# Performance work log

Measured on AMD Instinct MI355X. Metric: run time of the kernel, lower is better.

Reference implementation:

```python
import jax, jax.numpy as jnp
import numpy as np

B, L, D = 2, 2048, 2048
N, K, H = 16, 8, 128
EPS = 1e-6
ROPE_THETA = 1000000
K_MASK = -2.3819763e+38


def rms_norm(x, w, eps=EPS):
    dtype = x.dtype
    rms = jnp.sqrt(jnp.mean(x.astype(jnp.float32) ** 2, axis=-1, keepdims=True) + eps)
    return (w * x / rms).astype(dtype)


def apply_rope(inputs, positions, head_dim, rope_theta=ROPE_THETA):
    # inputs: [B, L, n, H], positions: [B, L]
    fraction = 2 * jnp.arange(0, head_dim // 2, dtype=jnp.float32) / head_dim
    timescale = rope_theta ** fraction  # [H/2]
    sinusoid = positions[..., jnp.newaxis] / timescale[jnp.newaxis, jnp.newaxis, :]  # [B,L,H/2]
    sinusoid = sinusoid[..., jnp.newaxis, :]  # [B,L,1,H/2]
    sin, cos = jnp.sin(sinusoid), jnp.cos(sinusoid)
    first, second = jnp.split(inputs, 2, axis=-1)
    out = jnp.concatenate([first * cos - second * sin, second * cos + first * sin], axis=-1)
    return out.astype(inputs.dtype)


def setup_inputs() -> dict:
    key = jax.random.key(0)
    ks = jax.random.split(key, 6)
    x = jax.random.normal(ks[0], (B, L, D), dtype=jnp.float32)
    position_ids = jnp.broadcast_to(jnp.arange(L, dtype=jnp.int32)[None, :], (B, L))
    # causal mask [B, L, S]
    attn_mask = jnp.broadcast_to(jnp.tril(jnp.ones((L, L), dtype=bool))[None], (B, L, L))
    wq = jax.random.normal(ks[1], (D, N, H), dtype=jnp.float32) * 0.02
    wk = jax.random.normal(ks[2], (D, K, H), dtype=jnp.float32) * 0.02
    wv = jax.random.normal(ks[3], (D, K, H), dtype=jnp.float32) * 0.02
    wo = jax.random.normal(ks[4], (N, H, D), dtype=jnp.float32) * 0.02
    q_norm_w = jnp.ones((H,), dtype=jnp.float32)
    k_norm_w = jnp.ones((H,), dtype=jnp.float32)
    return {"x": x, "position_ids": position_ids, "attn_mask": attn_mask,
            "wq": wq, "wk": wk, "wv": wv, "wo": wo,
            "q_norm_w": q_norm_w, "k_norm_w": k_norm_w}


def reference(x, position_ids, attn_mask, wq, wk, wv, wo, q_norm_w, k_norm_w):
    scale = H ** (-0.5)
    q = jnp.einsum('BLD,DNH->BLNH', x, wq)  # [B,L,N,H]
    k = jnp.einsum('BSD,DKH->BSKH', x, wk)  # [B,S,K,H]
    v = jnp.einsum('BSD,DKH->BSKH', x, wv)
    q = rms_norm(q, q_norm_w)
    k = rms_norm(k, k_norm_w)
    q = apply_rope(q, position_ids, H)
    k = apply_rope(k, position_ids, H)
    b, l, n, h = q.shape
    s = k.shape[1]
    kk = k.shape[2]
    q = q.reshape((b, l, kk, n // kk, h))
    attn = jnp.einsum('BLKGH,BSKH->BKGLS', q, k) * scale
    attn = attn.reshape((b, n, l, s))
    attn = jnp.where(jnp.expand_dims(attn_mask, -3), attn, K_MASK)
    attn = jax.nn.softmax(attn.astype(jnp.float32), axis=-1).astype(k.dtype)
    attn = attn.reshape((b, kk, n // kk, l, s))
    qkv = jnp.einsum('BKGLS,BSKH->BLKGH', attn, v).reshape((b, l, n, h))
    out = jnp.einsum('BLNH,NHD->BLD', qkv, wo)
    return out
```

## Files before the change

### kernel.cpp

```cpp
#include <hip/hip_runtime.h>
#include <hip/hip_bf16.h>

#define B_ 2
#define L_ 2048
#define D_ 2048
#define NH_ 16
#define KH_ 8
#define HD_ 128

typedef __attribute__((ext_vector_type(8))) short short8;
typedef __attribute__((ext_vector_type(4))) short short4v;
typedef __attribute__((ext_vector_type(4))) float floatx4;

__device__ __forceinline__ unsigned short f2bf(float f) {
  unsigned u = __float_as_uint(f);
  unsigned r = (u + 0x7fffu + ((u >> 16) & 1u)) >> 16;
  return (unsigned short)r;
}
__device__ __forceinline__ float bf2f(unsigned short h) {
  return __uint_as_float(((unsigned)h) << 16);
}
__device__ __forceinline__ unsigned pack_bf16x2(float a, float b) {
  __hip_bfloat162 h = __float22bfloat162_rn(make_float2(a, b));
  return *reinterpret_cast<unsigned*>(&h);
}
__device__ __forceinline__ void gl_lds16(const void* g, void* l) {
  __builtin_amdgcn_global_load_lds(
      (const __attribute__((address_space(1))) unsigned int*)g,
      (__attribute__((address_space(3))) unsigned int*)l, 16, 0, 0);
}
__device__ __forceinline__ void barrier_lds_only() {
  asm volatile("s_waitcnt lgkmcnt(0)" ::: "memory");
  __builtin_amdgcn_s_barrier();
}

__global__ __launch_bounds__(256) void prep1(const float* __restrict__ x,
                                             const float* __restrict__ wq,
                                             const float* __restrict__ wk,
                                             const float* __restrict__ wv,
                                             const float* __restrict__ wo,
                                             unsigned short* __restrict__ xb,
                                             unsigned short* __restrict__ wqkv_t,
                                             unsigned short* __restrict__ wo_t) {
  int id = blockIdx.x;
  int t = threadIdx.x;
  if (id < 8192) {
    long i = ((long)id * 256 + t) * 4;
    float4 v = *(const float4*)(x + i);
    ushort4 o;
    o.x = f2bf(v.x); o.y = f2bf(v.y); o.z = f2bf(v.z); o.w = f2bf(v.w);
    *(ushort4*)(xb + i) = o;
    return;
  }
  id -= 8192;
  __shared__ float tile[32][33];
  const float* in;
  unsigned short* out;
  int C, sh;
  if (id < 4096) {
    in = wq; out = wqkv_t; C = 2048; sh = 6;
  } else if (id < 6144) {
    in = wk; out = wqkv_t + 2048L * 2048; C = 1024; sh = 5; id -= 4096;
  } else if (id < 8192) {
    in = wv; out = wqkv_t + 3072L * 2048; C = 1024; sh = 5; id -= 6144;
  } else {
    in = wo; out = wo_t; C = 2048; sh = 6; id -= 8192;
  }
  int c0 = (id & ((1 << sh) - 1)) * 32, r0 = (id >> sh) * 32;
  int tx = t & 31, ty = t >> 5;
#pragma unroll
  for (int i = 0; i < 4; i++)
    tile[ty + i * 8][tx] = in[(long)(r0 + ty + i * 8) * C + c0 + tx];
  __syncthreads();
#pragma unroll
  for (int i = 0; i < 4; i++) {
    int oc = ty + i * 8;
    out[(long)(c0 + oc) * 2048 + r0 + tx] = f2bf(tile[tx][oc]);
  }
}

__global__ __launch_bounds__(256) void prep2(const unsigned short* __restrict__ qkv,
                                             const int* __restrict__ pos,
                                             const float* __restrict__ qw,
                                             const float* __restrict__ kw,
                                             unsigned short* __restrict__ qo,
                                             unsigned short* __restrict__ ko,
                                             unsigned short* __restrict__ vT) {
  int id = blockIdx.x;
  int t = threadIdx.x;
  if (id < 24576) {
    const int lane = t & 63, w = t >> 6;
    const int gid = id * 4 + w;
    const int row = gid / 24;
    const int hd = gid - row * 24;
    const int b = row >> 11, l = row & 2047;
    const unsigned short* src = qkv + (long)row * 4096 + hd * 128;
    float x0 = bf2f(src[lane]);
    float x1 = bf2f(src[lane + 64]);
    float ss = x0 * x0 + x1 * x1;
#pragma unroll
    for (int off = 32; off; off >>= 1) ss += __shfl_xor(ss, off);
    float inv = 1.0f / sqrtf(ss * (1.0f / 128.0f) + 1e-6f);
    const float* nw = (hd < 16) ? qw : kw;
    x0 = nw[lane] * x0 * inv;
    x1 = nw[lane + 64] * x1 * inv;
    float p = (float)pos[row];
    float ang = p * exp2f((float)lane * -0.31143075889f);
    float s, c;
    sincosf(ang, &s, &c);
    float o0 = x0 * c - x1 * s;
    float o1 = x1 * c + x0 * s;
    unsigned short* dst;
    if (hd < 16) {
      const float QSC = 0.08838834764831845f * 1.4426950408889634f;
      o0 *= QSC;
      o1 *= QSC;
      dst = qo + (((long)b * NH_ + hd) * L_ + l) * HD_;
    } else {
      dst = ko + (((long)b * KH_ + (hd - 16)) * L_ + l) * HD_;
    }
    dst[lane] = f2bf(o0);
    dst[lane + 64] = f2bf(o1);
    return;
  }
  id -= 24576;
  __shared__ unsigned short tile[32][33];
  int l0 = (id & 63) * 32, h0 = ((id >> 6) & 3) * 32;
  int bk = id >> 8;
  int b = bk >> 3, kh = bk & 7;
  int tx = t & 31, ty = t >> 5;
  const unsigned short* src = qkv + (long)b * L_ * 4096 + 3072 + kh * 128;
#pragma unroll
  for (int i = 0; i < 4; i++)
    tile[ty + i * 8][tx] = src[(long)(l0 + ty + i * 8) * 4096 + h0 + tx];
  __syncthreads();
  unsigned short* dst = vT + (long)bk * HD_ * L_;
#pragma unroll
  for (int i = 0; i < 4; i++)
    dst[(long)(h0 + ty + i * 8) * L_ + l0 + tx] = tile[tx][ty + i * 8];
}

template <int MODE>
__global__ __launch_bounds__(256, 3) void gemm128(const unsigned short* __restrict__ A,
                                                  const unsigned short* __restrict__ Bt,
                                                  void* __restrict__ C,
                                                  int M, int N, int K) {
  __shared__ unsigned short As[128 * 64];
  __shared__ unsigned short Bs[128 * 64];
  const int t = threadIdx.x;
  const int lane = t & 63, w = t >> 6;
  const int wy = w >> 1, wx = w & 1;
  const int col = lane & 15, quad = lane >> 4;
  const long m0 = (long)blockIdx.y * 128, n0 = (long)blockIdx.x * 128;
  floatx4 acc[4][4];
#pragma unroll
  for (int i = 0; i < 4; i++)
#pragma unroll
    for (int j = 0; j < 4; j++) acc[i][j] = (floatx4)0.0f;
  const int rs = t >> 3, bs = t & 7;
  for (int kt = 0; kt < K; kt += 64) {
#pragma unroll
    for (int i = 0; i < 4; i++) {
      int r = i * 32 + rs;
      gl_lds16(A + (m0 + r) * (long)K + kt + ((bs ^ (r & 7)) << 3),
               &As[(i * 32 + w * 8) * 64]);
      gl_lds16(Bt + (n0 + r) * (long)K + kt + ((bs ^ (r & 7)) << 3),
               &Bs[(i * 32 + w * 8) * 64]);
    }
    __syncthreads();
#pragma unroll
    for (int ks = 0; ks < 2; ks++) {
      short8 af[4], bf[4];
#pragma unroll
      for (int mi = 0; mi < 4; mi++) {
        int row = wy * 64 + mi * 16 + col;
        int blk = ks * 4 + quad;
        af[mi] = *(const short8*)&As[row * 64 + ((blk ^ (row & 7)) << 3)];
      }
#pragma unroll
      for (int ni = 0; ni < 4; ni++) {
        int row = wx * 64 + ni * 16 + col;
        int blk = ks * 4 + quad;
        bf[ni] = *(const short8*)&Bs[row * 64 + ((blk ^ (row & 7)) << 3)];
      }
#pragma unroll
      for (int mi = 0; mi < 4; mi++)
#pragma unroll
        for (int ni = 0; ni < 4; ni++)
          acc[mi][ni] = __builtin_amdgcn_mfma_f32_16x16x32_bf16(af[mi], bf[ni],
                                                                acc[mi][ni], 0, 0, 0);
    }
    __syncthreads();
  }
#pragma unroll
  for (int mi = 0; mi < 4; mi++)
#pragma unroll
    for (int r = 0; r < 4; r++) {
      long row = m0 + wy * 64 + mi * 16 + quad * 4 + r;
#pragma unroll
      for (int ni = 0; ni < 4; ni++) {
        long cg = n0 + wx * 64 + ni * 16 + col;
        float val = acc[mi][ni][r];
        if (MODE == 1)
          ((unsigned short*)C)[row * N + cg] = f2bf(val);
        else
          ((float*)C)[row * N + cg] = val;
      }
    }
}

template <int MODE>
__global__ __launch_bounds__(512, 2) void gemm256(const unsigned short* __restrict__ A,
                                                  const unsigned short* __restrict__ Bt,
                                                  void* __restrict__ C,
                                                  int M, int N, int K) {
  __shared__ unsigned short As[2][256 * 64];
  __shared__ unsigned short Bs[2][256 * 64];
  const int t = threadIdx.x;
  const int lane = t & 63, w = t >> 6;
  const int wy = w >> 2, wx = w & 3;
  const int col = lane & 15, quad = lane >> 4;
  const long m0 = (long)blockIdx.y * 256, n0 = (long)blockIdx.x * 256;
  const int rs = t >> 3, bs = t & 7;
  const int nt = K >> 6;

#define SA256(bufi, Tt, h)                                                      \
  gl_lds16(A + (m0 + (h) * 64 + rs) * (long)K + (long)(Tt) * 64 +               \
               ((bs ^ (rs & 7)) << 3),                                          \
           &As[bufi][((h) * 64 + w * 8) * 64])
#define SB256(bufi, Tt, h)                                                      \
  gl_lds16(Bt + (n0 + (h) * 64 + rs) * (long)K + (long)(Tt) * 64 +              \
                ((bs ^ (rs & 7)) << 3),                                         \
           &Bs[bufi][((h) * 64 + w * 8) * 64])

  floatx4 acc[8][4];
#pragma unroll
  for (int i = 0; i < 8; i++)
#pragma unroll
    for (int j = 0; j < 4; j++) acc[i][j] = (floatx4)0.0f;

  SA256(0, 0, 0); SA256(0, 0, 1); SA256(0, 0, 2); SA256(0, 0, 3);
  SB256(0, 0, 0); SB256(0, 0, 1); SB256(0, 0, 2); SB256(0, 0, 3);
  SB256(1, 1, 0); SB256(1, 1, 1); SB256(1, 1, 2); SB256(1, 1, 3);
  asm volatile("s_waitcnt vmcnt(4)" ::: "memory");
  __builtin_amdgcn_s_barrier();

  for (int T = 0; T < nt; ++T) {
    const int c = T & 1;
    const unsigned short* Ac = As[c];
    const unsigned short* Bc = Bs[c];
    short8 a[4][2], b[4][2];

#pragma unroll
    for (int mi = 0; mi < 4; mi++)
#pragma unroll
      for (int ks = 0; ks < 2; ks++) {
        int row = wy * 128 + mi * 16 + col;
        a[mi][ks] = *(const short8*)&Ac[row * 64 + (((ks * 4 + quad) ^ (row & 7)) << 3)];
      }
#pragma unroll
    for (int ni = 0; ni < 2; ni++)
#pragma unroll
      for (int ks = 0; ks < 2; ks++) {
        int row = wx * 64 + ni * 16 + col;
        b[ni][ks] = *(const short8*)&Bc[row * 64 + (((ks * 4 + quad) ^ (row & 7)) << 3)];
      }
    if (T + 1 < nt) { SA256(c ^ 1, T + 1, 0); SA256(c ^ 1, T + 1, 2); }
    __builtin_amdgcn_s_barrier();
    asm volatile("s_waitcnt lgkmcnt(0)" ::: "memory");
    __builtin_amdgcn_s_setprio(1);
#pragma unroll
    for (int mi = 0; mi < 4; mi++)
#pragma unroll
      for (int ni = 0; ni < 2; ni++)
#pragma unroll
        for (int ks = 0; ks < 2; ks++)
          acc[mi][ni] = __builtin_amdgcn_mfma_f32_16x16x32_bf16(a[mi][ks], b[ni][ks],
                                                                acc[mi][ni], 0, 0, 0);
    __builtin_amdgcn_s_setprio(0);
    __builtin_amdgcn_s_barrier();

#pragma unroll
    for (int ni = 2; ni < 4; ni++)
#pragma unroll
      for (int ks = 0; ks < 2; ks++) {
        int row = wx * 64 + ni * 16 + col;
        b[ni][ks] = *(const short8*)&Bc[row * 64 + (((ks * 4 + quad) ^ (row & 7)) << 3)];
      }
    if (T + 1 < nt) { SA256(c ^ 1, T + 1, 1); SA256(c ^ 1, T + 1, 3); }
    __builtin_amdgcn_s_barrier();
    asm volatile("s_waitcnt lgkmcnt(0)" ::: "memory");
    __builtin_amdgcn_s_setprio(1);
#pragma unroll
    for (int mi = 0; mi < 4; mi++)
#pragma unroll
      for (int ni = 2; ni < 4; ni++)
#pragma unroll
        for (int ks = 0; ks < 2; ks++)
          acc[mi][ni] = __builtin_amdgcn_mfma_f32_16x16x32_bf16(a[mi][ks], b[ni][ks],
                                                                acc[mi][ni], 0, 0, 0);
    __builtin_amdgcn_s_setprio(0);
    __builtin_amdgcn_s_barrier();

#pragma unroll
    for (int mi = 0; mi < 4; mi++)
#pragma unroll
      for (int ks = 0; ks < 2; ks++) {
        int row = wy * 128 + (mi + 4) * 16 + col;
        a[mi][ks] = *(const short8*)&Ac[row * 64 + (((ks * 4 + quad) ^ (row & 7)) << 3)];
      }
    if (T + 2 < nt) { SB256(c, T + 2, 0); SB256(c, T + 2, 1); }
    __builtin_amdgcn_s_barrier();
    asm volatile("s_waitcnt lgkmcnt(0)" ::: "memory");
    __builtin_amdgcn_s_setprio(1);
#pragma unroll
    for (int mi = 0; mi < 4; mi++)
#pragma unroll
      for (int ni = 0; ni < 2; ni++)
#pragma unroll
        for (int ks = 0; ks < 2; ks++)
          acc[mi + 4][ni] = __builtin_amdgcn_mfma_f32_16x16x32_bf16(a[mi][ks], b[ni][ks],
                                                                    acc[mi + 4][ni], 0, 0, 0);
    __builtin_amdgcn_s_setprio(0);
    __builtin_amdgcn_s_barrier();

    if (T + 2 < nt) { SB256(c, T + 2, 2); SB256(c, T + 2, 3); }
    __builtin_amdgcn_s_setprio(1);
#pragma unroll
    for (int mi = 0; mi < 4; mi++)
#pragma unroll
      for (int ni = 2; ni < 4; ni++)
#pragma unroll
        for (int ks = 0; ks < 2; ks++)
          acc[mi + 4][ni] = __builtin_amdgcn_mfma_f32_16x16x32_bf16(a[mi][ks], b[ni][ks],
                                                                    acc[mi + 4][ni], 0, 0, 0);
    __builtin_amdgcn_s_setprio(0);
    if (T + 1 < nt) {
      if (T >= nt - 2)
        asm volatile("s_waitcnt vmcnt(0)" ::: "memory");
      else
        asm volatile("s_waitcnt vmcnt(4)" ::: "memory");
      __builtin_amdgcn_s_barrier();
    }
  }
#undef SA256
#undef SB256

#pragma unroll
  for (int mi = 0; mi < 8; mi++)
#pragma unroll
    for (int r = 0; r < 4; r++) {
      long row = m0 + wy * 128 + mi * 16 + quad * 4 + r;
#pragma unroll
      for (int ni = 0; ni < 4; ni++) {
        long cg = n0 + wx * 64 + ni * 16 + col;
        float val = acc[mi][ni][r];
        if (MODE == 1)
          ((unsigned short*)C)[row * N + cg] = f2bf(val);
        else
          ((float*)C)[row * N + cg] = val;
      }
    }
}

__global__ __launch_bounds__(256, 2) void flash(const unsigned short* __restrict__ Q,
                                                const unsigned short* __restrict__ Kg,
                                                const unsigned short* __restrict__ VT,
                                                unsigned short* __restrict__ Og) {
  __shared__ unsigned short Ks[64 * 128];
  __shared__ unsigned short Vs[128 * 64];
  __shared__ unsigned short Ps[128 * 72];
  const int n = blockIdx.y, b = blockIdx.z;
  const int qt = b ? (15 - blockIdx.x) : blockIdx.x;
  const int t = threadIdx.x, lane = t & 63, w = t >> 6;
  const int col = lane & 15, quad = lane >> 4;
  const int kvh = n >> 1;
  const unsigned short* kb = Kg + ((long)b * KH_ + kvh) * L_ * HD_;
  const unsigned short* vtb = VT + ((long)b * KH_ + kvh) * HD_ * L_;
  const int l0 = qt * 128;
  const int steps = 2 * qt + 2;
  const unsigned short* qb = Q + (((long)b * NH_ + n) * L_ + l0) * HD_;

  const int rK = t >> 4, blkK = t & 15;
  const int rV = t >> 3, blkV = t & 7;

  short8 qf[2][4];
#pragma unroll
  for (int mi = 0; mi < 2; mi++)
#pragma unroll
    for (int ks = 0; ks < 4; ks++)
      qf[mi][ks] = *(const short8*)(qb + (w * 32 + mi * 16 + col) * 128 + ks * 32 + quad * 8);

  floatx4 o[2][8];
#pragma unroll
  for (int mi = 0; mi < 2; mi++)
#pragma unroll
    for (int nf = 0; nf < 8; nf++) o[mi][nf] = (floatx4)0.0f;
  float lrowA[2] = {0.0f, 0.0f}, lrowB[2] = {0.0f, 0.0f};

  {
#pragma unroll
    for (int i = 0; i < 4; i++) {
      int r = i * 16 + rK;
      int gblk = (blkK & 8) | ((blkK ^ r) & 7);
      gl_lds16(kb + (long)r * 128 + gblk * 8, &Ks[(i * 16 + w * 4) * 128]);
    }
#pragma unroll
    for (int j = 0; j < 4; j++) {
      int r = j * 32 + rV;
      int gblk = (blkV ^ r) & 7;
      gl_lds16(vtb + (long)r * L_ + gblk * 8, &Vs[(j * 32 + w * 8) * 64]);
    }
  }
  __syncthreads();

  short8 kpre[4], vpre[4];
  if (steps > 1) {
    const int s0n = 64;
#pragma unroll
    for (int i = 0; i < 4; i++) {
      int r = i * 16 + rK;
      int gblk = (blkK & 8) | ((blkK ^ r) & 7);
      kpre[i] = *(const short8*)(kb + (long)(s0n + r) * 128 + gblk * 8);
    }
#pragma unroll
    for (int j = 0; j < 4; j++) {
      int r = j * 32 + rV;
      int gblk = (blkV ^ r) & 7;
      vpre[j] = *(const short8*)(vtb + (long)r * L_ + s0n + gblk * 8);
    }
  }

  for (int st = 0; st < steps; st++) {
    const int s0 = st * 64;

    floatx4 sa[2][4];
#pragma unroll
    for (int mi = 0; mi < 2; mi++)
#pragma unroll
      for (int sf = 0; sf < 4; sf++) sa[mi][sf] = (floatx4)0.0f;
#pragma unroll
    for (int ks = 0; ks < 4; ks++) {
      short8 bf[4];
#pragma unroll
      for (int sf = 0; sf < 4; sf++) {
        int srow = sf * 16 + col;
        int blk = ks * 4 + quad;
        bf[sf] = *(const short8*)&Ks[srow * 128 + (((blk & 8) | ((blk ^ srow) & 7)) << 3)];
      }
#pragma unroll
      for (int mi = 0; mi < 2; mi++)
#pragma unroll
        for (int sf = 0; sf < 4; sf++)
          sa[mi][sf] = __builtin_amdgcn_mfma_f32_16x16x32_bf16(bf[sf], qf[mi][ks],
                                                               sa[mi][sf], 0, 0, 0);
    }

    if (st >= steps - 2) {
#pragma unroll
      for (int mi = 0; mi < 2; mi++) {
        int lg = l0 + w * 32 + mi * 16 + col;
#pragma unroll
        for (int sf = 0; sf < 4; sf++)
#pragma unroll
          for (int r = 0; r < 4; r++) {
            int sg = s0 + sf * 16 + quad * 4 + r;
            if (sg > lg) sa[mi][sf][r] = -3.0e38f;
          }
      }
    }

#pragma unroll
    for (int mi = 0; mi < 2; mi++)
#pragma unroll
      for (int sf = 0; sf < 4; sf++) {
        float p0 = exp2f(sa[mi][sf][0] - 17.0f);
        float p1 = exp2f(sa[mi][sf][1] - 17.0f);
        float p2 = exp2f(sa[mi][sf][2] - 17.0f);
        float p3 = exp2f(sa[mi][sf][3] - 17.0f);
        lrowA[mi] += p0 + p1;
        lrowB[mi] += p2 + p3;
        uint2 pk;
        pk.x = pack_bf16x2(p0, p1);
        pk.y = pack_bf16x2(p2, p3);
        *(uint2*)&Ps[(w * 32 + mi * 16 + col) * 72 + sf * 16 + quad * 4] = pk;
      }

#pragma unroll
    for (int ks = 0; ks < 2; ks++) {
      short8 pf[2];
#pragma unroll
      for (int mi = 0; mi < 2; mi++)
        pf[mi] = *(const short8*)&Ps[(w * 32 + mi * 16 + col) * 72 + ks * 32 + quad * 8];
      short8 vf[8];
#pragma unroll
      for (int nf = 0; nf < 8; nf++) {
        int h = nf * 16 + col;
        int blk = ks * 4 + quad;
        vf[nf] = *(const short8*)&Vs[h * 64 + ((blk ^ (h & 7)) << 3)];
      }
#pragma unroll
      for (int mi = 0; mi < 2; mi++)
#pragma unroll
        for (int nf = 0; nf < 8; nf++)
          o[mi][nf] = __builtin_amdgcn_mfma_f32_16x16x32_bf16(pf[mi], vf[nf],
                                                              o[mi][nf], 0, 0, 0);
    }

    barrier_lds_only();
    if (st + 1 < steps) {
#pragma unroll
      for (int i = 0; i < 4; i++) {
        int r = i * 16 + rK;
        *(short8*)&Ks[r * 128 + blkK * 8] = kpre[i];
      }
#pragma unroll
      for (int j = 0; j < 4; j++) {
        int r = j * 32 + rV;
        *(short8*)&Vs[r * 64 + blkV * 8] = vpre[j];
      }
      barrier_lds_only();
      if (st + 2 < steps) {
        const int s0n = (st + 2) * 64;
#pragma unroll
        for (int i = 0; i < 4; i++) {
          int r = i * 16 + rK;
          int gblk = (blkK & 8) | ((blkK ^ r) & 7);
          kpre[i] = *(const short8*)(kb + (long)(s0n + r) * 128 + gblk * 8);
        }
#pragma unroll
        for (int j = 0; j < 4; j++) {
          int r = j * 32 + rV;
          int gblk = (blkV ^ r) & 7;
          vpre[j] = *(const short8*)(vtb + (long)r * L_ + s0n + gblk * 8);
        }
      }
    }
  }

#pragma unroll
  for (int mi = 0; mi < 2; mi++) {
    float s = lrowA[mi] + lrowB[mi];
    s += __shfl_xor(s, 16);
    s += __shfl_xor(s, 32);
#pragma unroll
    for (int r = 0; r < 4; r++) {
      float inv = 1.0f / __shfl(s, quad * 4 + r);
      int lg = l0 + w * 32 + mi * 16 + quad * 4 + r;
      unsigned short* dst = Og + (((long)b * L_ + lg) * NH_ + n) * HD_;
#pragma unroll
      for (int nf = 0; nf < 8; nf++)
        dst[nf * 16 + col] = f2bf(o[mi][nf][r] * inv);
    }
  }
}

extern "C" void kernel_launch(void* const* d_in, const int* in_sizes, int n_in,
                              void* d_out, int out_size, void* d_ws, size_t ws_size,
                              hipStream_t stream) {
  const float* x = (const float*)d_in[0];
  const int* pos = (const int*)d_in[1];
  const float* wq = (const float*)d_in[3];
  const float* wk = (const float*)d_in[4];
  const float* wv = (const float*)d_in[5];
  const float* wo = (const float*)d_in[6];
  const float* qnw = (const float*)d_in[7];
  const float* knw = (const float*)d_in[8];
  float* out = (float*)d_out;

  char* ws = (char*)d_ws;
  unsigned short* xb     = (unsigned short*)(ws + 0);
  unsigned short* wqkv_t = (unsigned short*)(ws + 16777216);
  unsigned short* wo_t   = (unsigned short*)(ws + 33554432);
  unsigned short* qkv    = (unsigned short*)(ws + 41943040);
  unsigned short* q      = (unsigned short*)(ws + 75497472);
  unsigned short* k      = (unsigned short*)(ws + 92274688);
  unsigned short* vT     = (unsigned short*)(ws + 100663296);
  unsigned short* ao     = (unsigned short*)(ws + 109051904);
  if (ws_size < 125829120) return;

  prep1<<<20480, 256, 0, stream>>>(x, wq, wk, wv, wo, xb, wqkv_t, wo_t);
  gemm256<1><<<dim3(16, 16), 512, 0, stream>>>(xb, wqkv_t, qkv, 4096, 4096, 2048);
  prep2<<<28672, 256, 0, stream>>>(qkv, pos, qnw, knw, q, k, vT);
  flash<<<dim3(16, NH_, B_), 256, 0, stream>>>(q, k, vT, ao);
  gemm128<0><<<dim3(16, 32), 256, 0, stream>>>(ao, wo_t, out, 4096, 2048, 2048);
}
```

Before: 349.8 us.

## Fuse QK RMS-norm, RoPE and V transpose into QKV GEMM epilogue

Removes the separate prep2 kernel by adding a MODE 2 epilogue to the QKV gemm256 kernel. The epilogue computes per-head RMS norms through an LDS partial-sum reduction, applies RoPE and the Q scale, and writes Q/K in head-major layout. It also transposes V through swizzled LDS directly into vT. This avoids writing and re-reading the full bf16 qkv intermediate and one launch, at the cost of a longer, barrier-heavy epilogue in the GEMM. The flash kernel's bf16 packing is also switched to a manual rounding helper.

```diff
diff --git a/kernel.cpp b/kernel.cpp
--- a/kernel.cpp
+++ b/kernel.cpp
@@ -1,5 +1,4 @@
 #include <hip/hip_runtime.h>
-#include <hip/hip_bf16.h>
 
 #define B_ 2
 #define L_ 2048
@@ -19,10 +18,6 @@
 }
 __device__ __forceinline__ float bf2f(unsigned short h) {
   return __uint_as_float(((unsigned)h) << 16);
-}
-__device__ __forceinline__ unsigned pack_bf16x2(float a, float b) {
-  __hip_bfloat162 h = __float22bfloat162_rn(make_float2(a, b));
-  return *reinterpret_cast<unsigned*>(&h);
 }
 __device__ __forceinline__ void gl_lds16(const void* g, void* l) {
   __builtin_amdgcn_global_load_lds(
@@ -79,67 +74,6 @@
   }
 }
 
-__global__ __launch_bounds__(256) void prep2(const unsigned short* __restrict__ qkv,
-                                             const int* __restrict__ pos,
-                                             const float* __restrict__ qw,
-                                             const float* __restrict__ kw,
-                                             unsigned short* __restrict__ qo,
-                                             unsigned short* __restrict__ ko,
-                                             unsigned short* __restrict__ vT) {
-  int id = blockIdx.x;
-  int t = threadIdx.x;
-  if (id < 24576) {
-    const int lane = t & 63, w = t >> 6;
-    const int gid = id * 4 + w;
-    const int row = gid / 24;
-    const int hd = gid - row * 24;
-    const int b = row >> 11, l = row & 2047;
-    const unsigned short* src = qkv + (long)row * 4096 + hd * 128;
-    float x0 = bf2f(src[lane]);
-    float x1 = bf2f(src[lane + 64]);
-    float ss = x0 * x0 + x1 * x1;
-#pragma unroll
-    for (int off = 32; off; off >>= 1) ss += __shfl_xor(ss, off);
-    float inv = 1.0f / sqrtf(ss * (1.0f / 128.0f) + 1e-6f);
-    const float* nw = (hd < 16) ? qw : kw;
-    x0 = nw[lane] * x0 * inv;
-    x1 = nw[lane + 64] * x1 * inv;
-    float p = (float)pos[row];
-    float ang = p * exp2f((float)lane * -0.31143075889f);
-    float s, c;
-    sincosf(ang, &s, &c);
-    float o0 = x0 * c - x1 * s;
-    float o1 = x1 * c + x0 * s;
-    unsigned short* dst;
-    if (hd < 16) {
-      const float QSC = 0.08838834764831845f * 1.4426950408889634f;
-      o0 *= QSC;
-      o1 *= QSC;
-      dst = qo + (((long)b * NH_ + hd) * L_ + l) * HD_;
-    } else {
-      dst = ko + (((long)b * KH_ + (hd - 16)) * L_ + l) * HD_;
-    }
-    dst[lane] = f2bf(o0);
-    dst[lane + 64] = f2bf(o1);
-    return;
-  }
-  id -= 24576;
-  __shared__ unsigned short tile[32][33];
-  int l0 = (id & 63) * 32, h0 = ((id >> 6) & 3) * 32;
-  int bk = id >> 8;
-  int b = bk >> 3, kh = bk & 7;
-  int tx = t & 31, ty = t >> 5;
-  const unsigned short* src = qkv + (long)b * L_ * 4096 + 3072 + kh * 128;
-#pragma unroll
-  for (int i = 0; i < 4; i++)
-    tile[ty + i * 8][tx] = src[(long)(l0 + ty + i * 8) * 4096 + h0 + tx];
-  __syncthreads();
-  unsigned short* dst = vT + (long)bk * HD_ * L_;
-#pragma unroll
-  for (int i = 0; i < 4; i++)
-    dst[(long)(h0 + ty + i * 8) * L_ + l0 + tx] = tile[tx][ty + i * 8];
-}
-
 template <int MODE>
 __global__ __launch_bounds__(256, 3) void gemm128(const unsigned short* __restrict__ A,
                                                   const unsigned short* __restrict__ Bt,
@@ -213,9 +147,14 @@
 __global__ __launch_bounds__(512, 2) void gemm256(const unsigned short* __restrict__ A,
                                                   const unsigned short* __restrict__ Bt,
                                                   void* __restrict__ C,
-                                                  int M, int N, int K) {
-  __shared__ unsigned short As[2][256 * 64];
-  __shared__ unsigned short Bs[2][256 * 64];
+                                                  int M, int N, int K,
+                                                  unsigned short* __restrict__ qptr,
+                                                  unsigned short* __restrict__ kptr,
+                                                  unsigned short* __restrict__ vTptr,
+                                                  const int* __restrict__ posp,
+                                                  const float* __restrict__ qwp,
+                                                  const float* __restrict__ kwp) {
+  __shared__ unsigned short SMu[4][256 * 64];
   const int t = threadIdx.x;
   const int lane = t & 63, w = t >> 6;
   const int wy = w >> 2, wx = w & 3;
@@ -227,11 +166,11 @@
 #define SA256(bufi, Tt, h)                                                      \
   gl_lds16(A + (m0 + (h) * 64 + rs) * (long)K + (long)(Tt) * 64 +               \
                ((bs ^ (rs & 7)) << 3),                                          \
-           &As[bufi][((h) * 64 + w * 8) * 64])
+           &SMu[bufi][((h) * 64 + w * 8) * 64])
 #define SB256(bufi, Tt, h)                                                      \
   gl_lds16(Bt + (n0 + (h) * 64 + rs) * (long)K + (long)(Tt) * 64 +              \
                 ((bs ^ (rs & 7)) << 3),                                         \
-           &Bs[bufi][((h) * 64 + w * 8) * 64])
+           &SMu[2 + (bufi)][((h) * 64 + w * 8) * 64])
 
   floatx4 acc[8][4];
 #pragma unroll
@@ -247,8 +186,8 @@
 
   for (int T = 0; T < nt; ++T) {
     const int c = T & 1;
-    const unsigned short* Ac = As[c];
-    const unsigned short* Bc = Bs[c];
+    const unsigned short* Ac = SMu[c];
+    const unsigned short* Bc = SMu[2 + c];
     short8 a[4][2], b[4][2];
 
 #pragma unroll
@@ -345,6 +284,114 @@
   }
 #undef SA256
 #undef SB256
+
+  if (MODE == 2) {
+    const int bx = blockIdx.x;
+    const int bb = (int)(m0 >> 11);
+    const int l0r = (int)(m0 & 2047);
+    __syncthreads();
+
+    if (bx >= 12) {
+      const int khb = (bx - 12) * 2;
+      unsigned short* Vt = (unsigned short*)SMu;
+#pragma unroll
+      for (int mi = 0; mi < 8; mi++)
+#pragma unroll
+        for (int ni = 0; ni < 4; ni++) {
+          int cc = wx * 64 + ni * 16 + col;
+          int rbase = wy * 128 + mi * 16 + quad * 4;
+          short4v pk;
+#pragma unroll
+          for (int r = 0; r < 4; r++) pk[r] = (short)f2bf(acc[mi][ni][r]);
+          *(short4v*)&Vt[cc * 256 + (rbase ^ ((cc & 15) << 4))] = pk;
+        }
+      __syncthreads();
+      for (int i = 0; i < 32; i++) {
+        int cc = w * 32 + i;
+        int hloc = cc & 127;
+        int khh = khb + (cc >> 7);
+        ushort4 v4 = *(const ushort4*)&Vt[cc * 256 + ((lane * 4) ^ ((cc & 15) << 4))];
+        *(ushort4*)&vTptr[(((long)bb * KH_ + khh) * HD_ + hloc) * (long)L_ + l0r + lane * 4] = v4;
+      }
+      return;
+    }
+
+    const bool isq = (bx < 8);
+    const float* nwp = isq ? qwp : kwp;
+    float* PART = (float*)SMu;
+#pragma unroll
+    for (int mi = 0; mi < 8; mi++)
+#pragma unroll
+      for (int r = 0; r < 4; r++) {
+        float s = acc[mi][0][r] * acc[mi][0][r] + acc[mi][1][r] * acc[mi][1][r] +
+                  acc[mi][2][r] * acc[mi][2][r] + acc[mi][3][r] * acc[mi][3][r];
+        s += __shfl_xor(s, 1);
+        s += __shfl_xor(s, 2);
+        s += __shfl_xor(s, 4);
+        s += __shfl_xor(s, 8);
+        if (col == 0)
+          PART[((wy * 128 + mi * 16 + quad * 4 + r) << 2) + wx] = s;
+      }
+    __syncthreads();
+    float inv[8][4];
+    {
+      const int wp = (wx >> 1) << 1;
+#pragma unroll
+      for (int mi = 0; mi < 8; mi++)
+#pragma unroll
+        for (int r = 0; r < 4; r++) {
+          int lr = wy * 128 + mi * 16 + quad * 4 + r;
+          float ss = PART[(lr << 2) + wp] + PART[(lr << 2) + wp + 1];
+          inv[mi][r] = 1.0f / sqrtf(ss * (1.0f / 128.0f) + 1e-6f);
+        }
+    }
+    __syncthreads();
+    float* plane = (float*)SMu;
+    const float nw0 = nwp[lane], nw1 = nwp[lane + 64];
+    const float QSC = 0.08838834764831845f * 1.4426950408889634f;
+    for (int hh = 0; hh < 2; hh++) {
+      if (wy == hh) {
+#pragma unroll
+        for (int mi = 0; mi < 8; mi++)
+#pragma unroll
+          for (int ni = 0; ni < 4; ni++) {
+            int cc = wx * 64 + ni * 16 + col;
+#pragma unroll
+            for (int r = 0; r < 4; r++)
+              plane[(mi * 16 + quad * 4 + r) * 256 + cc] = acc[mi][ni][r] * inv[mi][r];
+          }
+      }
+      __syncthreads();
+      for (int i = 0; i < 16; i++) {
+        int lr = w * 16 + i;
+        int lg = l0r + hh * 128 + lr;
+        float x0a = plane[lr * 256 + lane];
+        float x1a = plane[lr * 256 + lane + 64];
+        float x0b = plane[lr * 256 + 128 + lane];
+        float x1b = plane[lr * 256 + 192 + lane];
+        float p = (float)posp[bb * L_ + lg];
+        float ang = p * exp2f((float)lane * -0.31143075889f);
+        float sv, cv;
+        sincosf(ang, &sv, &cv);
+        x0a *= nw0; x1a *= nw1; x0b *= nw0; x1b *= nw1;
+        float o0a = x0a * cv - x1a * sv, o1a = x1a * cv + x0a * sv;
+        float o0b = x0b * cv - x1b * sv, o1b = x1b * cv + x0b * sv;
+        unsigned short* d0;
+        if (isq) {
+          o0a *= QSC; o1a *= QSC; o0b *= QSC; o1b *= QSC;
+          d0 = qptr + (((long)bb * NH_ + bx * 2) * L_ + lg) * HD_;
+        } else {
+          d0 = kptr + (((long)bb * KH_ + (bx - 8) * 2) * L_ + lg) * HD_;
+        }
+        d0[lane] = f2bf(o0a);
+        d0[lane + 64] = f2bf(o1a);
+        d0[(long)L_ * HD_ + lane] = f2bf(o0b);
+        d0[(long)L_ * HD_ + lane + 64] = f2bf(o1b);
+      }
+      __syncthreads();
+    }
+    return;
+  }
 
 #pragma unroll
   for (int mi = 0; mi < 8; mi++)
@@ -433,7 +480,6 @@
 
   for (int st = 0; st < steps; st++) {
     const int s0 = st * 64;
-
     floatx4 sa[2][4];
 #pragma unroll
     for (int mi = 0; mi < 2; mi++)
@@ -480,10 +526,12 @@
         float p3 = exp2f(sa[mi][sf][3] - 17.0f);
         lrowA[mi] += p0 + p1;
         lrowB[mi] += p2 + p3;
-        uint2 pk;
-        pk.x = pack_bf16x2(p0, p1);
-        pk.y = pack_bf16x2(p2, p3);
-        *(uint2*)&Ps[(w * 32 + mi * 16 + col) * 72 + sf * 16 + quad * 4] = pk;
+        short4v pk;
+        pk[0] = (short)f2bf(p0);
+        pk[1] = (short)f2bf(p1);
+        pk[2] = (short)f2bf(p2);
+        pk[3] = (short)f2bf(p3);
+        *(short4v*)&Ps[(w * 32 + mi * 16 + col) * 72 + sf * 16 + quad * 4] = pk;
       }
 
 #pragma unroll
@@ -572,7 +620,6 @@
   unsigned short* xb     = (unsigned short*)(ws + 0);
   unsigned short* wqkv_t = (unsigned short*)(ws + 16777216);
   unsigned short* wo_t   = (unsigned short*)(ws + 33554432);
-  unsigned short* qkv    = (unsigned short*)(ws + 41943040);
   unsigned short* q      = (unsigned short*)(ws + 75497472);
   unsigned short* k      = (unsigned short*)(ws + 92274688);
   unsigned short* vT     = (unsigned short*)(ws + 100663296);
@@ -580,8 +627,8 @@
   if (ws_size < 125829120) return;
 
   prep1<<<20480, 256, 0, stream>>>(x, wq, wk, wv, wo, xb, wqkv_t, wo_t);
-  gemm256<1><<<dim3(16, 16), 512, 0, stream>>>(xb, wqkv_t, qkv, 4096, 4096, 2048);
-  prep2<<<28672, 256, 0, stream>>>(qkv, pos, qnw, knw, q, k, vT);
+  gemm256<2><<<dim3(16, 16), 512, 0, stream>>>(xb, wqkv_t, nullptr, 4096, 4096, 2048,
+                                               q, k, vT, pos, qnw, knw);
   flash<<<dim3(16, NH_, B_), 256, 0, stream>>>(q, k, vT, ao);
   gemm128<0><<<dim3(16, 32), 256, 0, stream>>>(ao, wo_t, out, 4096, 2048, 2048);
 }
```

New measurement: 336.1 us (median of 2 runs). 1.04x faster.
